# Kernel tuning notes

Hardware: AMD Instinct MI355X
Metric: run time of the kernel (lower is better)

The kernel has to match this reference:

```python
import jax, jax.numpy as jnp
import numpy as np

N, E, F_IN, H = 100000, 3200000, 256, 32

def gcn_conv(x, src, dst, w, W, b):
    # PyG GCNConv with edge weights and added self-loops (weight 1), symmetric norm
    xw = x @ W                                                # [N, H]
    deg = jax.ops.segment_sum(w, dst, num_segments=N) + 1.0   # includes self-loop
    dis = jax.lax.rsqrt(deg)                                  # deg >= 1, safe
    norm = dis[src] * w * dis[dst]                            # [E]
    agg = jax.ops.segment_sum(norm[:, None] * xw[src], dst, num_segments=N)
    agg = agg + (dis * dis)[:, None] * xw                     # self-loop term
    return agg + b


def setup_inputs() -> dict:
    key = jax.random.key(0)
    ks = jax.random.split(key, 20)
    z = lambda n: jnp.zeros((n,), jnp.float32)
    p = lambda i, shape, s: jax.random.normal(ks[i], shape, jnp.float32) * s
    return {
        "x": jax.random.normal(ks[0], (N, F_IN), jnp.float32),
        "edge_index": jax.random.randint(ks[1], (2, E), 0, N),
        "edge_weight": jax.random.uniform(ks[2], (E,), jnp.float32),
        "prev_hidden_state": jax.random.normal(ks[3], (N, H), jnp.float32),
        # GCNConv weights (stored [in, out]) + post-aggregation biases
        "W_z": p(4, (F_IN, H), 0.05), "b_z": z(H),
        "W_r": p(5, (F_IN, H), 0.05), "b_r": z(H),
        "W_h": p(6, (F_IN, H), 0.05), "b_h": z(H),
        # GRU gate linears Linear(2H, H), stored [2H, H]
        "Lz_W": p(7, (2 * H, H), 0.1), "Lz_b": z(H),
        "Lr_W": p(8, (2 * H, H), 0.1), "Lr_b": z(H),
        "Lh_W": p(9, (2 * H, H), 0.1), "Lh_b": z(H),
        # readout Linear(H, 1)
        "head_W": p(10, (H, 1), 0.1), "head_b": z(1),
    }


def reference(x, edge_index, edge_weight, prev_hidden_state,
              W_z, b_z, W_r, b_r, W_h, b_h,
              Lz_W, Lz_b, Lr_W, Lr_b, Lh_W, Lh_b,
              head_W, head_b):
    src, dst = edge_index[0], edge_index[1]
    Hp = prev_hidden_state
    Z = jax.nn.sigmoid(
        jnp.concatenate([gcn_conv(x, src, dst, edge_weight, W_z, b_z), Hp], 1) @ Lz_W + Lz_b)
    R = jax.nn.sigmoid(
        jnp.concatenate([gcn_conv(x, src, dst, edge_weight, W_r, b_r), Hp], 1) @ Lr_W + Lr_b)
    H_tilde = jnp.tanh(
        jnp.concatenate([gcn_conv(x, src, dst, edge_weight, W_h, b_h), Hp * R], 1) @ Lh_W + Lh_b)
    h = Z * Hp + (1.0 - Z) * H_tilde
    y = jax.nn.relu(h) @ head_W + head_b
    return (y, h)
```

## Files before the change

kernel.cpp:

```cpp
#include <hip/hip_runtime.h>
#include <math.h>

#define N_NODES 100000
#define F_INDIM 256
#define NB 391
#define BCAP 9216
#define CNT_BLOCKS 521
#define K1_BLOCKS 3647

__device__ __forceinline__ unsigned bf16pack(float a, float b) {
  unsigned ua = __float_as_uint(a);
  ua += 0x7FFFu + ((ua >> 16) & 1u);
  unsigned ub = __float_as_uint(b);
  ub += 0x7FFFu + ((ub >> 16) & 1u);
  return (ub & 0xFFFF0000u) | (ua >> 16);
}
__device__ __forceinline__ float lo16(unsigned v) { return __uint_as_float(v << 16); }
__device__ __forceinline__ float hi16(unsigned v) { return __uint_as_float(v & 0xFFFF0000u); }

__global__ __launch_bounds__(256) void gemm_bin(
    const float* __restrict__ x,
    const float* __restrict__ Wz, const float* __restrict__ Wr, const float* __restrict__ Wh,
    unsigned* __restrict__ XWb,
    const int* __restrict__ ei, const float* __restrict__ w,
    int* __restrict__ bucketCursor, uint2* __restrict__ staged, int E) {
  __shared__ float smem[8192];
  const int t = threadIdx.x;
  const int m = blockIdx.x % 7;
  if (m == 0) {
    int* lc    = (int*)smem;
    int* lbase = (int*)smem + 512;
    for (int i = t; i < NB; i += 256) lc[i] = 0;
    __syncthreads();
    const int base = (blockIdx.x / 7) * 6144;
#pragma unroll
    for (int i = 0; i < 24; i++) {
      int e = base + i * 256 + t;
      if (e < E) atomicAdd(&lc[((unsigned)ei[E + e]) >> 8], 1);
    }
    __syncthreads();
    for (int i = t; i < NB; i += 256) {
      int c = lc[i];
      lbase[i] = c ? atomicAdd(&bucketCursor[i], c) : 0;
    }
    __syncthreads();
    for (int i = t; i < NB; i += 256) lc[i] = 0;
    __syncthreads();
#pragma unroll
    for (int i = 0; i < 24; i++) {
      int e = base + i * 256 + t;
      if (e < E) {
        unsigned dst = (unsigned)ei[E + e];
        int b = dst >> 8;
        int r = lbase[b] + atomicAdd(&lc[b], 1);
        if (r < BCAP)
          staged[(size_t)b * BCAP + r] =
              make_uint2((unsigned)ei[e] | ((dst & 255u) << 17), __float_as_uint(w[e]));
      }
    }
    return;
  }
  float (*xs)[64]  = (float(*)[64])smem;
  float (*wsz)[32] = (float(*)[32])(smem + 2048);
  float (*wsr)[32] = (float(*)[32])(smem + 4096);
  float (*wsh)[32] = (float(*)[32])(smem + 6144);
  const int gid = (blockIdx.x / 7) * 6 + (m - 1);
  const int row0 = gid * 32;
  if (row0 >= N_NODES) return;
  const int cg = t & 31;
  const int rg = (t >> 5) * 4;
  float acc[4][3] = {};
  for (int k0 = 0; k0 < 256; k0 += 64) {
#pragma unroll
    for (int i = 0; i < 8; i++) {
      int l = t + 256 * i;
      int r = l >> 6, kk = l & 63;
      xs[r][kk] = x[(size_t)(row0 + r) * F_INDIM + k0 + kk];
    }
#pragma unroll
    for (int i = 0; i < 8; i++) {
      int l = t + 256 * i;
      int kk = l >> 5, c = l & 31;
      wsz[kk][c] = Wz[(k0 + kk) * 32 + c];
      wsr[kk][c] = Wr[(k0 + kk) * 32 + c];
      wsh[kk][c] = Wh[(k0 + kk) * 32 + c];
    }
    __syncthreads();
#pragma unroll 4
    for (int kk = 0; kk < 64; kk++) {
      float wz = wsz[kk][cg], wr = wsr[kk][cg], wh = wsh[kk][cg];
#pragma unroll
      for (int r = 0; r < 4; r++) {
        float xv = xs[rg + r][kk];
        acc[r][0] = fmaf(xv, wz, acc[r][0]);
        acc[r][1] = fmaf(xv, wr, acc[r][1]);
        acc[r][2] = fmaf(xv, wh, acc[r][2]);
      }
    }
    __syncthreads();
  }
#pragma unroll
  for (int r = 0; r < 4; r++) {
    int row = row0 + rg + r;
#pragma unroll
    for (int g2 = 0; g2 < 3; g2++) {
      float other = __shfl_xor(acc[r][g2], 1);
      if ((cg & 1) == 0)
        XWb[(size_t)row * 48 + g2 * 16 + (cg >> 1)] = bf16pack(acc[r][g2], other);
    }
  }
}

__global__ __launch_bounds__(256) void finalize(
    const uint2* __restrict__ staged, const int* __restrict__ bucketCursor,
    uint2* __restrict__ e2, int* __restrict__ rowstart, int* __restrict__ cntA,
    float* __restrict__ dis) {
  __shared__ int fc[256];
  __shared__ float fd[256];
  __shared__ int fscan[256];
  __shared__ int fcur[256];
  const int t = threadIdx.x;
  const int b = blockIdx.x;
  const size_t lo = (size_t)b * BCAP;
  int M = bucketCursor[b]; if (M > BCAP) M = BCAP;
  fc[t] = 0; fd[t] = 0.f;
  __syncthreads();
  for (int i = t; i < M; i += 256) {
    uint2 ed = staged[lo + i];
    int fl = (ed.x >> 17) & 255;
    atomicAdd(&fc[fl], 1);
    atomicAdd(&fd[fl], __uint_as_float(ed.y));
  }
  __syncthreads();
  int v = fc[t];
  fscan[t] = v;
  __syncthreads();
  for (int off = 1; off < 256; off <<= 1) {
    int xv = (t >= off) ? fscan[t - off] : 0;
    __syncthreads();
    fscan[t] += xv;
    __syncthreads();
  }
  int excl = fscan[t] - v;
  int node = (b << 8) + t;
  if (node < N_NODES) {
    rowstart[node] = (int)lo + excl;
    cntA[node] = v;
    dis[node] = rsqrtf(fd[t] + 1.0f);
  }
  fcur[t] = excl;
  __syncthreads();
  for (int i = t; i < M; i += 256) {
    uint2 ed = staged[lo + i];
    int fl = (ed.x >> 17) & 255;
    int p = atomicAdd(&fcur[fl], 1);
    e2[lo + p] = make_uint2(ed.x & 0x1FFFFu, ed.y);
  }
}

#define FMA8(vv, nn)                                              \
  a0 = fmaf(nn, lo16(vv.x), a0); a1 = fmaf(nn, hi16(vv.x), a1);   \
  a2 = fmaf(nn, lo16(vv.y), a2); a3 = fmaf(nn, hi16(vv.y), a3);   \
  a4 = fmaf(nn, lo16(vv.z), a4); a5 = fmaf(nn, hi16(vv.z), a5);   \
  a6 = fmaf(nn, lo16(vv.w), a6); a7 = fmaf(nn, hi16(vv.w), a7);

__global__ __launch_bounds__(256, 6) void gru_gather(
    const uint2* __restrict__ e2, const int* __restrict__ rowstart,
    const int* __restrict__ cnt, const unsigned* __restrict__ XWb,
    const float* __restrict__ dis, const float* __restrict__ Hp,
    const float* __restrict__ bz, const float* __restrict__ br, const float* __restrict__ bh,
    const float* __restrict__ LzW, const float* __restrict__ Lzb,
    const float* __restrict__ LrW, const float* __restrict__ Lrb,
    const float* __restrict__ LhW, const float* __restrict__ Lhb,
    const float* __restrict__ hW, const float* __restrict__ hb,
    float* __restrict__ outY, float* __restrict__ outH, int N) {
  __shared__ unsigned sLz[1024], sLr[1024], sLh[1024];
  __shared__ float aggTmp[4][5][96];
  __shared__ float sb96[96];
  __shared__ float sLzb[32], sLrb[32], sLhb[32], shW[32];
  __shared__ float2 sg2[4][48];
  __shared__ float shp[4][32], shr[4][32];
  __shared__ float shb;
  const int t = threadIdx.x;
  for (int i = t; i < 1024; i += 256) {
    int jj = i & 31, k2 = i >> 5;
    sLz[i] = bf16pack(LzW[(2 * k2) * 32 + jj], LzW[(2 * k2 + 1) * 32 + jj]);
    sLr[i] = bf16pack(LrW[(2 * k2) * 32 + jj], LrW[(2 * k2 + 1) * 32 + jj]);
    sLh[i] = bf16pack(LhW[(2 * k2) * 32 + jj], LhW[(2 * k2 + 1) * 32 + jj]);
  }
  if (t < 32) {
    sb96[t] = bz[t]; sb96[32 + t] = br[t]; sb96[64 + t] = bh[t];
    sLzb[t] = Lzb[t]; sLrb[t] = Lrb[t]; sLhb[t] = Lhb[t]; shW[t] = hW[t];
  }
  if (t == 0) shb = hb[0];
  __syncthreads();
  const int ws = t >> 6;
  const int l = t & 63;
  const int lp = (l < 48) ? l : 47;
  const int j = l & 31;
  const int half = l >> 5;
  const int sl = (l < 60) ? (l / 12) : 4;
  const int q  = (l < 60) ? (l % 12) : 11;
  const float* sgf = (const float*)&sg2[ws][0];
  int wid = blockIdx.x * 4 + ws;
  int nw = gridDim.x * 4;
  for (int n = wid; n < N; n += nw) {
    const int start = rowstart[n];
    const int c = cnt[n];
    const float d = dis[n];
    float a0 = 0.f, a1 = 0.f, a2 = 0.f, a3 = 0.f;
    float a4 = 0.f, a5 = 0.f, a6 = 0.f, a7 = 0.f;
    for (int e0 = 0; e0 < c; e0 += 60) {
      int srcv = 0; float pw = 0.f;
      if (l < 60 && e0 + l < c) {
        uint2 ed = e2[start + e0 + l];
        srcv = (int)ed.x;
        pw = __uint_as_float(ed.y) * dis[srcv];
      }
      int mm = c - e0; if (mm > 60) mm = 60;
      for (int k0 = 0; k0 < mm; k0 += 10) {
        int iA = k0 + sl, iB = k0 + 5 + sl;
        int sA = __shfl(srcv, iA), sB = __shfl(srcv, iB);
        float nA = __shfl(pw, iA), nB = __shfl(pw, iB);
        uint4 vA = *(const uint4*)(XWb + sA * 48 + (q << 2));
        uint4 vB = *(const uint4*)(XWb + sB * 48 + (q << 2));
        FMA8(vA, nA);
        FMA8(vB, nB);
      }
    }
    if (l < 60) {
      float4* dst4 = (float4*)&aggTmp[ws][sl][q * 8];
      dst4[0] = make_float4(a0, a1, a2, a3);
      dst4[1] = make_float4(a4, a5, a6, a7);
    }
    float g0 = 0.f, g1 = 0.f;
#pragma unroll
    for (int ss = 0; ss < 5; ss++) {
      float2 v2 = *(const float2*)&aggTmp[ws][ss][2 * lp];
      g0 += v2.x; g1 += v2.y;
    }
    g0 *= d; g1 *= d;
    {
      unsigned v = XWb[n * 48 + lp];
      float d2 = d * d;
      g0 = fmaf(d2, lo16(v), g0) + sb96[2 * lp];
      g1 = fmaf(d2, hi16(v), g1) + sb96[2 * lp + 1];
    }
    if (l < 48) sg2[ws][l] = make_float2(g0, g1);
    float hpj = 0.f;
    if (l < 32) { hpj = Hp[(size_t)n * 32 + l]; shp[ws][l] = hpj; }
    const unsigned* Wm = half ? sLr : sLz;
    const float* gsel = half ? (sgf + 32) : sgf;
    float val = half ? sLrb[j] : sLzb[j];
#pragma unroll
    for (int k2 = 0; k2 < 16; k2++) {
      unsigned wv = Wm[k2 * 32 + j];
      val = fmaf(gsel[2 * k2],     lo16(wv), val);
      val = fmaf(gsel[2 * k2 + 1], hi16(wv), val);
    }
#pragma unroll
    for (int k2 = 16; k2 < 32; k2++) {
      unsigned wv = Wm[k2 * 32 + j];
      val = fmaf(shp[ws][2 * k2 - 32], lo16(wv), val);
      val = fmaf(shp[ws][2 * k2 - 31], hi16(wv), val);
    }
    float gate = 1.f / (1.f + __expf(-val));
    if (half) shr[ws][j] = shp[ws][j] * gate;
    float s = half ? 0.f : sLhb[j];
#pragma unroll
    for (int k2 = 0; k2 < 16; k2++) {
      int kk2 = half ? (k2 + 16) : k2;
      unsigned wv = sLh[kk2 * 32 + j];
      float x0 = half ? shr[ws][2 * k2]     : sgf[64 + 2 * k2];
      float x1 = half ? shr[ws][2 * k2 + 1] : sgf[64 + 2 * k2 + 1];
      s = fmaf(x0, lo16(wv), s);
      s = fmaf(x1, hi16(wv), s);
    }
    s += __shfl_xor(s, 32);
    if (!half) {
      float ht = tanhf(s);
      float h = gate * hpj + (1.f - gate) * ht;
      outH[(size_t)n * 32 + j] = h;
      float cacc = fmaxf(h, 0.f) * shW[j];
#pragma unroll
      for (int off = 16; off > 0; off >>= 1) cacc += __shfl_xor(cacc, off, 32);
      if (j == 0) outY[n] = cacc + shb;
    }
  }
}

extern "C" void kernel_launch(void* const* d_in, const int* in_sizes, int n_in,
                              void* d_out, int out_size, void* d_ws, size_t ws_size,
                              hipStream_t stream) {
  const float* x    = (const float*)d_in[0];
  const int*   ei   = (const int*)d_in[1];
  const float* w    = (const float*)d_in[2];
  const float* Hp   = (const float*)d_in[3];
  const float* Wz   = (const float*)d_in[4];
  const float* bz   = (const float*)d_in[5];
  const float* Wr   = (const float*)d_in[6];
  const float* br   = (const float*)d_in[7];
  const float* Wh   = (const float*)d_in[8];
  const float* bh   = (const float*)d_in[9];
  const float* LzW  = (const float*)d_in[10];
  const float* Lzb  = (const float*)d_in[11];
  const float* LrW  = (const float*)d_in[12];
  const float* Lrb  = (const float*)d_in[13];
  const float* LhW  = (const float*)d_in[14];
  const float* Lhb  = (const float*)d_in[15];
  const float* hW   = (const float*)d_in[16];
  const float* hb   = (const float*)d_in[17];

  const int N = N_NODES;
  const int E = in_sizes[2];

  char* p = (char*)d_ws;
  unsigned* XWb   = (unsigned*)p;  p += (size_t)(N * 48 + 64) * 4;
  uint2*    staged= (uint2*)p;     p += (size_t)NB * BCAP * 8;
  uint2*    e2    = (uint2*)p;     p += (size_t)NB * BCAP * 8;
  int* rowstart   = (int*)p;       p += (size_t)N * 4;
  int* cnt        = (int*)p;       p += (size_t)N * 4;
  float* dis      = (float*)p;     p += (size_t)N * 4;
  int* bucketCursor = (int*)p;     p += (NB + 1) * 4;

  float* outY = (float*)d_out;
  float* outH = outY + N;

  hipMemsetAsync(bucketCursor, 0, (NB + 1) * sizeof(int), stream);

  gemm_bin<<<K1_BLOCKS, 256, 0, stream>>>(x, Wz, Wr, Wh, XWb, ei, w,
                                          bucketCursor, staged, E);
  finalize<<<NB, 256, 0, stream>>>(staged, bucketCursor, e2, rowstart, cnt, dis);
  gru_gather<<<1536, 256, 0, stream>>>(e2, rowstart, cnt, XWb, dis, Hp,
                                       bz, br, bh,
                                       LzW, Lzb, LrW, Lrb, LhW, Lhb,
                                       hW, hb, outY, outH, N);
}
```

Baseline: 283.6 us.

## Compute the XW projection with bf16 MFMA and rebalance the binning blocks

Replaces the scalar FP32 FMA tiling of the x @ [Wz|Wr|Wh] projection with bf16 MFMA 16x16x32 instructions. x is read straight from global memory as float4 and packed to bf16 in registers. The three weight matrices are transposed into LDS as bf16 once per block, and each 512-thread block now covers 128 rows. The edge-binning work is regrouped to two of every five blocks, each running 512 threads. The aim is to cut the ALU and LDS cost of the projection so the kernel is limited by x bandwidth. The trade-offs are that x is rounded to bf16 before the multiply, which lowers precision, and that every block redoes the weight transpose.

```diff
diff --git a/kernel.cpp b/kernel.cpp
--- a/kernel.cpp
+++ b/kernel.cpp
@@ -5,8 +5,6 @@
 #define F_INDIM 256
 #define NB 391
 #define BCAP 9216
-#define CNT_BLOCKS 521
-#define K1_BLOCKS 3647
 
 __device__ __forceinline__ unsigned bf16pack(float a, float b) {
   unsigned ua = __float_as_uint(a);
@@ -18,37 +16,41 @@
 __device__ __forceinline__ float lo16(unsigned v) { return __uint_as_float(v << 16); }
 __device__ __forceinline__ float hi16(unsigned v) { return __uint_as_float(v & 0xFFFF0000u); }
 
-__global__ __launch_bounds__(256) void gemm_bin(
+using bf16x8 = __attribute__((ext_vector_type(8))) short;
+using f32x4  = __attribute__((ext_vector_type(4))) float;
+
+__global__ __launch_bounds__(512) void gemm_bin(
     const float* __restrict__ x,
     const float* __restrict__ Wz, const float* __restrict__ Wr, const float* __restrict__ Wh,
     unsigned* __restrict__ XWb,
     const int* __restrict__ ei, const float* __restrict__ w,
     int* __restrict__ bucketCursor, uint2* __restrict__ staged, int E) {
-  __shared__ float smem[8192];
+  __shared__ unsigned smem[12672];
   const int t = threadIdx.x;
-  const int m = blockIdx.x % 7;
-  if (m == 0) {
+  const int m = blockIdx.x % 5;
+  if (m < 2) {
     int* lc    = (int*)smem;
     int* lbase = (int*)smem + 512;
-    for (int i = t; i < NB; i += 256) lc[i] = 0;
-    __syncthreads();
-    const int base = (blockIdx.x / 7) * 6144;
-#pragma unroll
-    for (int i = 0; i < 24; i++) {
-      int e = base + i * 256 + t;
+    if (t < NB) lc[t] = 0;
+    __syncthreads();
+    const int bid = (blockIdx.x / 5) * 2 + m;
+    const int base = bid * 6144;
+#pragma unroll
+    for (int i = 0; i < 12; i++) {
+      int e = base + i * 512 + t;
       if (e < E) atomicAdd(&lc[((unsigned)ei[E + e]) >> 8], 1);
     }
     __syncthreads();
-    for (int i = t; i < NB; i += 256) {
-      int c = lc[i];
-      lbase[i] = c ? atomicAdd(&bucketCursor[i], c) : 0;
-    }
-    __syncthreads();
-    for (int i = t; i < NB; i += 256) lc[i] = 0;
-    __syncthreads();
-#pragma unroll
-    for (int i = 0; i < 24; i++) {
-      int e = base + i * 256 + t;
+    if (t < NB) {
+      int c = lc[t];
+      lbase[t] = c ? atomicAdd(&bucketCursor[t], c) : 0;
+    }
+    __syncthreads();
+    if (t < NB) lc[t] = 0;
+    __syncthreads();
+#pragma unroll
+    for (int i = 0; i < 12; i++) {
+      int e = base + i * 512 + t;
       if (e < E) {
         unsigned dst = (unsigned)ei[E + e];
         int b = dst >> 8;
@@ -60,53 +62,60 @@
     }
     return;
   }
-  float (*xs)[64]  = (float(*)[64])smem;
-  float (*wsz)[32] = (float(*)[32])(smem + 2048);
-  float (*wsr)[32] = (float(*)[32])(smem + 4096);
-  float (*wsh)[32] = (float(*)[32])(smem + 6144);
-  const int gid = (blockIdx.x / 7) * 6 + (m - 1);
-  const int row0 = gid * 32;
+  const int gid = (blockIdx.x / 5) * 3 + (m - 2);
+  const int row0 = gid * 128;
   if (row0 >= N_NODES) return;
-  const int cg = t & 31;
-  const int rg = (t >> 5) * 4;
-  float acc[4][3] = {};
-  for (int k0 = 0; k0 < 256; k0 += 64) {
-#pragma unroll
-    for (int i = 0; i < 8; i++) {
-      int l = t + 256 * i;
-      int r = l >> 6, kk = l & 63;
-      xs[r][kk] = x[(size_t)(row0 + r) * F_INDIM + k0 + kk];
-    }
-#pragma unroll
-    for (int i = 0; i < 8; i++) {
-      int l = t + 256 * i;
-      int kk = l >> 5, c = l & 31;
-      wsz[kk][c] = Wz[(k0 + kk) * 32 + c];
-      wsr[kk][c] = Wr[(k0 + kk) * 32 + c];
-      wsh[kk][c] = Wh[(k0 + kk) * 32 + c];
-    }
-    __syncthreads();
-#pragma unroll 4
-    for (int kk = 0; kk < 64; kk++) {
-      float wz = wsz[kk][cg], wr = wsr[kk][cg], wh = wsh[kk][cg];
-#pragma unroll
-      for (int r = 0; r < 4; r++) {
-        float xv = xs[rg + r][kk];
-        acc[r][0] = fmaf(xv, wz, acc[r][0]);
-        acc[r][1] = fmaf(xv, wr, acc[r][1]);
-        acc[r][2] = fmaf(xv, wh, acc[r][2]);
+  ushort* sWt = (ushort*)smem;
+  {
+    const float* Ws[3] = {Wz, Wr, Wh};
+#pragma unroll
+    for (int mm = 0; mm < 3; mm++) {
+      const float* Wp = Ws[mm];
+      for (int i = t; i < 8192; i += 512) {
+        int k = i >> 5, c = i & 31;
+        unsigned uv = __float_as_uint(Wp[i]);
+        uv += 0x7FFFu + ((uv >> 16) & 1u);
+        sWt[(mm * 32 + c) * 264 + k] = (ushort)(uv >> 16);
       }
     }
-    __syncthreads();
-  }
-#pragma unroll
-  for (int r = 0; r < 4; r++) {
-    int row = row0 + rg + r;
-#pragma unroll
-    for (int g2 = 0; g2 < 3; g2++) {
-      float other = __shfl_xor(acc[r][g2], 1);
-      if ((cg & 1) == 0)
-        XWb[(size_t)row * 48 + g2 * 16 + (cg >> 1)] = bf16pack(acc[r][g2], other);
+  }
+  __syncthreads();
+  const int wv = t >> 6;
+  const int l = t & 63;
+  const int nl = l & 15;
+  const int kg = l >> 4;
+  int arow = row0 + wv * 16 + nl;
+  int arowc = arow < N_NODES ? arow : N_NODES - 1;
+  f32x4 acc[6];
+#pragma unroll
+  for (int c = 0; c < 6; c++) acc[c] = (f32x4){0.f, 0.f, 0.f, 0.f};
+  const float* xrow = x + (size_t)arowc * F_INDIM + kg * 8;
+#pragma unroll
+  for (int ks = 0; ks < 8; ks++) {
+    float4 xa = *(const float4*)(xrow + ks * 32);
+    float4 xb = *(const float4*)(xrow + ks * 32 + 4);
+    uint4 au;
+    au.x = bf16pack(xa.x, xa.y);
+    au.y = bf16pack(xa.z, xa.w);
+    au.z = bf16pack(xb.x, xb.y);
+    au.w = bf16pack(xb.z, xb.w);
+    bf16x8 af = *(bf16x8*)&au;
+#pragma unroll
+    for (int c = 0; c < 6; c++) {
+      const ushort* bp = sWt + (c * 16 + nl) * 264 + ks * 32 + kg * 8;
+      bf16x8 bf = *(const bf16x8*)bp;
+      acc[c] = __builtin_amdgcn_mfma_f32_16x16x32_bf16(af, bf, acc[c], 0, 0, 0);
+    }
+  }
+#pragma unroll
+  for (int c = 0; c < 6; c++) {
+#pragma unroll
+    for (int r = 0; r < 4; r++) {
+      float v = acc[c][r];
+      float o = __shfl_xor(v, 1);
+      int orow = row0 + wv * 16 + kg * 4 + r;
+      if ((nl & 1) == 0 && orow < N_NODES)
+        XWb[(size_t)orow * 48 + c * 8 + (nl >> 1)] = bf16pack(v, o);
     }
   }
 }
@@ -328,8 +337,8 @@
 
   hipMemsetAsync(bucketCursor, 0, (NB + 1) * sizeof(int), stream);
 
-  gemm_bin<<<K1_BLOCKS, 256, 0, stream>>>(x, Wz, Wr, Wh, XWb, ei, w,
-                                          bucketCursor, staged, E);
+  gemm_bin<<<1305, 512, 0, stream>>>(x, Wz, Wr, Wh, XWb, ei, w,
+                                     bucketCursor, staged, E);
   finalize<<<NB, 256, 0, stream>>>(staged, bucketCursor, e2, rowstart, cnt, dis);
   gru_gather<<<1536, 256, 0, stream>>>(e2, rowstart, cnt, XWb, dis, Hp,
                                        bz, br, bh,
```

Result: faster. 232.0 us (-18.2%).
